# Kernel tuning notes

Hardware: AMD Instinct MI355X
Metric: run time of the kernel (lower is better)

Reference implementation:

```python
import jax, jax.numpy as jnp
import numpy as np


def _glorot(key, shape):
    lim = np.sqrt(6.0 / (shape[-2] + shape[-1])).astype(np.float32)
    return jax.random.uniform(key, shape, jnp.float32, -lim, lim)


def setup_inputs() -> dict:
    key = jax.random.key(0)
    B, F, K, L = 8192, 256, 32768, 4
    H = 2 * F          # CouplingLayer(feat_size, feat_size * 2) hidden width
    half = F // 2      # affine coupling transforms half the features
    ks = jax.random.split(key, 6)
    return {
        "inputs": jax.random.normal(ks[0], (B, F), jnp.float32),
        "W1": _glorot(ks[1], (L, half, H)),
        "b1": jnp.zeros((L, H), jnp.float32),
        "Ws": _glorot(ks[2], (L, H, half)),
        "bs": jnp.zeros((L, half), jnp.float32),
        "Wt": _glorot(ks[3], (L, H, half)),
        "bt": jnp.zeros((L, half), jnp.float32),
        "prior": _glorot(ks[4], (K, F)),  # VQ codebook, GlorotUniform init as in source
    }


def _forward_flow(x, W1, b1, Ws, bs, Wt, bt):
    """Stack of affine coupling layers; returns (y, log|det J|) per sample."""
    L = W1.shape[0]
    jac = jnp.zeros((x.shape[0],), x.dtype)
    for l in range(L):  # small fixed layer count
        xa, xb = jnp.split(x, 2, axis=1)                 # [B, F/2] each
        h = jax.nn.relu(xa @ W1[l] + b1[l])              # [B, 2F]
        s_raw = h @ Ws[l] + bs[l]                        # [B, F/2]
        s = s_raw if l == L - 1 else jnp.tanh(s_raw)     # last layer: tf.identity
        t = h @ Wt[l] + bt[l]
        yb = xb * jnp.exp(s) + t
        jac = jac + jnp.sum(s, axis=1)
        x = jnp.concatenate([yb, xa], axis=1)            # swap halves for mixing
    return x, jac


def reference(inputs, W1, b1, Ws, bs, Wt, bt, prior):
    sg = jax.lax.stop_gradient
    x, jac = _forward_flow(inputs, W1, b1, Ws, bs, Wt, bt)   # [B, F], [B]
    # pairwise squared distance to codebook: [B, K]
    na = jnp.sum(x * x, axis=1, keepdims=True)               # [B, 1]
    nb = jnp.sum(prior * prior, axis=1)[None, :]             # [1, K]
    d = jnp.maximum(na - 2.0 * (x @ prior.T) + nb, 0.0)      # [B, K]
    target_ind = jnp.argmin(d, axis=1)                       # [B]
    target = prior[target_ind]                               # gather, [B, F]
    loss_1 = jnp.mean(jnp.sum((x - sg(target)) ** 2, axis=1) / 2)
    loss_2 = jnp.mean(jnp.sum((sg(x) - target) ** 2, axis=1) / 2)
    loss = loss_1 + 0.25 * loss_2 - jnp.mean(jac)
    return x, loss
```

## Files before the change

kernel.cpp:

```cpp
#include <hip/hip_runtime.h>
#include <hip/hip_fp8.h>
#include <stdint.h>

#define NB     8192
#define NF     256
#define NHALF  128
#define NHID   512
#define NLAY   4
#define NK     32768

#define SX     (1.0f / 16.0f)
#define SP     (256.0f)

typedef __attribute__((ext_vector_type(8))) short bf16x8;
typedef __attribute__((ext_vector_type(4))) float f32x4;
typedef __attribute__((ext_vector_type(2))) long i64x2;

static __device__ __forceinline__ unsigned short f2bf(float f) {
  union { float f; unsigned int u; } v; v.f = f;
  return (unsigned short)((v.u + 0x7FFFu + ((v.u >> 16) & 1u)) >> 16);
}
static __device__ __forceinline__ float bf2f(unsigned short u) {
  union { unsigned int u; float f; } v; v.u = ((unsigned int)u) << 16; return v.f;
}
static __device__ __forceinline__ unsigned char f2fp8(float f) {
  __hip_fp8_e4m3 q(f);
  return (unsigned char)q.__x;
}
static __device__ __forceinline__ float fp82f(unsigned char b) {
  __hip_fp8_e4m3 q; q.__x = b; return (float)q;
}
static __device__ __forceinline__ int kperm(int k) {
  return ((k >> 3) & 3) * 64 + ((k >> 5) << 3) + (k & 7);
}

static __device__ __forceinline__ void load_lds16(const void* g, void* l) {
  __builtin_amdgcn_global_load_lds(
      (const __attribute__((address_space(1))) unsigned int*)g,
      (__attribute__((address_space(3))) unsigned int*)l, 16, 0, 0);
}

static __device__ __forceinline__ unsigned long long packsi(float v, int idx) {
  unsigned int b = __float_as_uint(v);
  b = (b & 0x80000000u) ? ~b : (b | 0x80000000u);
  return ((unsigned long long)b << 32) | (unsigned int)(~(unsigned int)idx);
}

static __device__ __forceinline__ float fast_tanh(float x) {
  const float xc = fminf(fmaxf(x, -15.f), 15.f);
  const float e2 = __expf(2.f * xc);
  return 1.f - 2.f / (e2 + 1.f);
}

static __device__ __forceinline__ int swadr(int kseg, int nrows, int row, int kin) {
  return (kseg * nrows + row) * 64 + (((kin >> 3) ^ (row & 7)) * 8) + (kin & 7);
}

__global__ __launch_bounds__(256, 2)
void flow_all(const float* __restrict__ in,
              const unsigned short* __restrict__ W1T,
              const unsigned short* __restrict__ W2I,
              const float* __restrict__ b1A,
              const float* __restrict__ bsA,
              const float* __restrict__ btA,
              float* __restrict__ xout,
              unsigned char* __restrict__ xf8,
              float* __restrict__ jac)
{
  __shared__ __align__(16) unsigned short Xb[2][16 * 128];
  __shared__ __align__(16) unsigned short Hs[16 * 64];
  __shared__ __align__(16) unsigned short Bs[2][8192];
  __shared__ float jlds[3][16];
  const int tid = threadIdx.x;
  const int lane = tid & 63, wave = tid >> 6;
  const int q = lane >> 4, c = lane & 15;
  const int m0 = blockIdx.x * 16;

  {
    const unsigned short* W1l = W1T;
#pragma unroll
    for (int u = 0; u < 4; u++) {
      const int chb = (u * 4 + wave) * 64;
      const int ch = chb + lane;
      const int kseg = ch >> 9, cs = ch & 511;
      const int row = cs >> 3, cc = (cs & 7) ^ (row & 7);
      load_lds16(W1l + (size_t)row * 128 + kseg * 64 + cc * 8, Bs[0] + chb * 8);
    }
  }

#pragma unroll
  for (int v = 0; v < 4; v++) {
    const int t4 = tid + v * 256;
    const int row = t4 >> 6, f4 = t4 & 63;
    const float4 d = *(const float4*)(in + (size_t)(m0 + row) * NF + f4 * 4);
    unsigned short* dst = Xb[f4 >> 5];
    const int feat = (f4 & 31) * 4;
    const float vals[4] = {d.x, d.y, d.z, d.w};
#pragma unroll
    for (int u = 0; u < 4; u++) {
      const int fe = feat + u;
      dst[swadr(fe >> 6, 16, row, fe & 63)] = f2bf(vals[u]);
    }
  }

  float jr[4] = {0.f, 0.f, 0.f, 0.f};
  bf16x8 af1[4];
  const f32x4 z = {0.f, 0.f, 0.f, 0.f};
  f32x4 acc2[4];

  for (int gs = 0; gs < 96; gs++) {
    __syncthreads();

    if (gs + 1 < 96) {
      const int g2 = gs + 1;
      const int l2 = g2 / 24, s2 = g2 % 24, nc2 = s2 / 3, t2 = s2 % 3;
      unsigned short* dst = Bs[g2 & 1];
      if (t2 == 0) {
        const unsigned short* W1l = W1T + (size_t)l2 * (NHID * NHALF) + (size_t)nc2 * 64 * 128;
#pragma unroll
        for (int u = 0; u < 4; u++) {
          const int chb = (u * 4 + wave) * 64;
          const int ch = chb + lane;
          const int kseg = ch >> 9, cs = ch & 511;
          const int row = cs >> 3, cc = (cs & 7) ^ (row & 7);
          load_lds16(W1l + (size_t)row * 128 + kseg * 64 + cc * 8, dst + chb * 8);
        }
      } else {
        const unsigned short* W2l = W2I + (size_t)l2 * (NF * NHID) + nc2 * 64 + (t2 - 1) * 32;
#pragma unroll
        for (int u = 0; u < 4; u++) {
          const int chb = (u * 4 + wave) * 64;
          const int ch = chb + lane;
          const int row = ch >> 2;
          const int cc = (ch & 3) ^ ((row >> 1) & 3);
          load_lds16(W2l + (size_t)row * NHID + cc * 8, dst + chb * 8);
        }
      }
    }

    const int l = gs / 24, s = gs % 24, nc8 = s / 3, typ = s % 3;
    const unsigned short* B = Bs[gs & 1];
    unsigned short* XA = Xb[l & 1];
    unsigned short* XB = Xb[1 - (l & 1)];

    if (typ == 0) {
      if (s == 0) {
#pragma unroll
        for (int kw = 0; kw < 4; kw++) {
          const int kch = kw * 4 + q;
          af1[kw] = *(const bf16x8*)(XA + ((kch >> 3) * 16 + c) * 64 +
                                     (((kch & 7) ^ (c & 7)) * 8));
        }
#pragma unroll
        for (int j = 0; j < 4; j++) acc2[j] = z;
      }
      f32x4 acc1 = z;
      const int rb = wave * 16 + c;
#pragma unroll
      for (int kw = 0; kw < 4; kw++) {
        const int kseg = kw >> 1, g = (kw & 1) * 4 + q;
        const bf16x8 bf = *(const bf16x8*)(B + (kseg * 64 + rb) * 64 + ((g ^ (rb & 7)) * 8));
        acc1 = __builtin_amdgcn_mfma_f32_16x16x32_bf16(af1[kw], bf, acc1, 0, 0, 0);
      }
      const int hc = wave * 16 + c;
      const float bb = b1A[l * NHID + nc8 * 64 + hc];
#pragma unroll
      for (int r = 0; r < 4; r++) {
        float v = acc1[r] + bb;
        v = v > 0.f ? v : 0.f;
        Hs[swadr(0, 16, 4 * q + r, hc)] = f2bf(v);
      }
    } else {
      const int half = typ - 1;
      const bf16x8 afh = *(const bf16x8*)(Hs + c * 64 + (((half * 4 + q) ^ (c & 7)) * 8));
#pragma unroll
      for (int j = 0; j < 4; j++) {
        const int rb = wave * 64 + 16 * j + c;
        const bf16x8 bf = *(const bf16x8*)(B + rb * 32 + ((q ^ ((rb >> 1) & 3)) * 8));
        acc2[j] = __builtin_amdgcn_mfma_f32_16x16x32_bf16(afh, bf, acc2[j], 0, 0, 0);
      }
    }

    if (s == 23) {
      const int parity = c & 1;
      const int lastl = (l == NLAY - 1);
      const float* bsl = bsA + l * NHALF;
      const float* btl = btA + l * NHALF;
#pragma unroll
      for (int j = 0; j < 4; j++) {
        const int col = wave * 64 + 16 * j + c;
#pragma unroll
        for (int r = 0; r < 4; r++) {
          const float val = acc2[j][r];
          const float oth = __shfl_xor(val, 1);
          if (!parity) {
            const int feat = col >> 1;
            float sv = val + bsl[feat];
            if (!lastl) sv = fast_tanh(sv);
            const float t = oth + btl[feat];
            const int row = 4 * q + r;
            const int xaddr = swadr(feat >> 6, 16, row, feat & 63);
            const float xb = bf2f(XB[xaddr]);
            const float yb = xb * __expf(sv) + t;
            jr[r] += sv;
            XB[xaddr] = f2bf(yb);
            if (l >= 2) {
              const int k = lastl ? feat : (NHALF + feat);
              const size_t grow = (size_t)(m0 + row) * NF;
              xout[grow + k] = yb;
              xf8[(size_t)(m0 + row) * 256 + kperm(k)] = f2fp8(yb * SX);
            }
          }
        }
      }
    }
  }

  float v0[4];
#pragma unroll
  for (int r = 0; r < 4; r++) {
    float v = jr[r];
    v += __shfl_xor(v, 1); v += __shfl_xor(v, 2);
    v += __shfl_xor(v, 4); v += __shfl_xor(v, 8);
    if (c == 0) {
      if (wave) jlds[wave - 1][4 * q + r] = v;
      else v0[r] = v;
    }
  }
  __syncthreads();
  if (wave == 0 && c == 0) {
#pragma unroll
    for (int r = 0; r < 4; r++) {
      const int row = 4 * q + r;
      jac[m0 + row] = v0[r] + jlds[0][row] + jlds[1][row] + jlds[2][row];
    }
  }
}

__global__ __launch_bounds__(256, 2)
void vq_argmax(const unsigned char* __restrict__ X8,
               const unsigned char* __restrict__ P8,
               const float* __restrict__ nbh,
               unsigned long long* __restrict__ gbest)
{
  __shared__ __align__(16) unsigned char Bs[64 * 256];
  const int tid = threadIdx.x;
  const int lane = tid & 63, wave = tid >> 6;
  const int y = blockIdx.x & 15;
  const int m0 = (blockIdx.x >> 4) * 256;
  const int q = lane >> 4, c = lane & 15;
  const int mw = m0 + wave * 64;

  long af[4][8];
#pragma unroll
  for (int i = 0; i < 4; i++) {
    const unsigned char* xr = X8 + (size_t)(mw + 16 * i + c) * 256 + q * 64;
#pragma unroll
    for (int kc2 = 0; kc2 < 4; kc2++) {
      const i64x2 v = *(const i64x2*)(xr + kc2 * 16);
      af[i][2 * kc2] = v.x; af[i][2 * kc2 + 1] = v.y;
    }
  }

  float bestv[16];
  int besti[16];
#pragma unroll
  for (int t = 0; t < 16; t++) { bestv[t] = -1e30f; besti[t] = 0; }

  for (int nt = 0; nt < 32; nt++) {
    const int n0 = y * 2048 + nt * 64;
    if (nt) __syncthreads();
#pragma unroll
    for (int u = 0; u < 4; u++) {
      const int chb = (u * 4 + wave) * 64;
      const int ch = chb + lane;
      const int row = ch >> 4, gslot = ch & 15;
      load_lds16(P8 + (size_t)(n0 + row) * 256 + (gslot ^ (row & 15)) * 16,
                 Bs + chb * 16);
    }
    __syncthreads();

    const f32x4 z = {0.f, 0.f, 0.f, 0.f};
    f32x4 acc[4][4];
#pragma unroll
    for (int i = 0; i < 4; i++)
#pragma unroll
      for (int j = 0; j < 4; j++) acc[i][j] = z;

#pragma unroll
    for (int kc2 = 0; kc2 < 4; kc2++) {
      const int g = q * 4 + kc2;
#pragma unroll
      for (int j = 0; j < 4; j++) {
        const int rb = 16 * j + c;
        const i64x2 b2 = *(const i64x2*)(Bs + rb * 256 + ((g ^ (rb & 15)) * 16));
#pragma unroll
        for (int i = 0; i < 4; i++) {
          acc[i][j] = __builtin_amdgcn_mfma_f32_16x16x32_fp8_fp8(af[i][2 * kc2],     b2.x, acc[i][j], 0, 0, 0);
          acc[i][j] = __builtin_amdgcn_mfma_f32_16x16x32_fp8_fp8(af[i][2 * kc2 + 1], b2.y, acc[i][j], 0, 0, 0);
        }
      }
    }

#pragma unroll
    for (int j = 0; j < 4; j++) {
      const int col = n0 + 16 * j + c;
      const float nb = nbh[col];
#pragma unroll
      for (int i = 0; i < 4; i++)
#pragma unroll
        for (int r = 0; r < 4; r++) {
          const float sc = acc[i][j][r] - nb;
          const int t = i * 4 + r;
          if (sc > bestv[t]) { bestv[t] = sc; besti[t] = col; }
        }
    }
  }

#pragma unroll
  for (int t = 0; t < 16; t++) {
    float lv = bestv[t]; int li = besti[t];
#pragma unroll
    for (int mk = 8; mk >= 1; mk >>= 1) {
      const float ov = __shfl_xor(lv, mk);
      const int oi = __shfl_xor(li, mk);
      if (ov > lv || (ov == lv && oi < li)) { lv = ov; li = oi; }
    }
    if (c == 0) {
      const int row = mw + 16 * (t >> 2) + q * 4 + (t & 3);
      atomicMax(&gbest[row], packsi(lv, li));
    }
  }
}

__global__ void prep_all(const float* __restrict__ W1,
                         const float* __restrict__ Ws,
                         const float* __restrict__ Wt,
                         const float* __restrict__ prior,
                         unsigned short* __restrict__ W1T,
                         unsigned short* __restrict__ W2I,
                         unsigned char* __restrict__ p8,
                         float* __restrict__ nbh,
                         unsigned long long* __restrict__ gbest,
                         float* __restrict__ accum)
{
  __shared__ float ts[64 * 65];
  const int bx = blockIdx.x;
  const int tid = threadIdx.x;
  if (bx < 2048) {
    const int k = bx * 16 + (tid >> 4);
    const int l16 = tid & 15;
    float s = 0.f;
#pragma unroll
    for (int v = 0; v < 4; v++) {
      const int off = (v * 16 + l16) * 4;
      const float4 d = *(const float4*)(prior + (size_t)k * NF + off);
      uchar4 o;
      o.x = f2fp8(d.x * SP); o.y = f2fp8(d.y * SP);
      o.z = f2fp8(d.z * SP); o.w = f2fp8(d.w * SP);
      *(uchar4*)(p8 + (size_t)k * 256 + kperm(off)) = o;
      const float q0 = fp82f(o.x), q1 = fp82f(o.y), q2 = fp82f(o.z), q3 = fp82f(o.w);
      s += q0 * q0 + q1 * q1 + q2 * q2 + q3 * q3;
    }
#pragma unroll
    for (int mk = 8; mk >= 1; mk >>= 1) s += __shfl_xor(s, mk);
    if (l16 == 0) nbh[k] = 0.5f * s * (SX / SP);
  } else if (bx < 2112) {
    const int job = bx - 2048;
    const int l = job >> 4, t = job & 15;
    const int k0 = (t >> 3) * 64, n0 = (t & 7) * 64;
    const float* src = W1 + (size_t)l * NHALF * NHID;
#pragma unroll
    for (int v = 0; v < 16; v++) {
      const int e = tid + v * 256;
      const int kk = e >> 6, nn = e & 63;
      ts[kk * 65 + nn] = src[(size_t)(k0 + kk) * NHID + n0 + nn];
    }
    __syncthreads();
    unsigned short* dst = W1T + (size_t)l * NHID * NHALF;
#pragma unroll
    for (int v = 0; v < 16; v++) {
      const int e = tid + v * 256;
      const int nn = e >> 6, kk = e & 63;
      dst[(size_t)(n0 + nn) * NHALF + k0 + kk] = f2bf(ts[kk * 65 + nn]);
    }
  } else if (bx < 2240) {
    const int job = bx - 2112;
    const int l = job >> 5, rem = job & 31;
    const int b = rem >> 4;
    const int k0 = ((rem >> 1) & 7) * 64;
    const int f0 = (rem & 1) * 64;
    const float* src = (b ? Wt : Ws) + (size_t)l * NHID * NHALF;
#pragma unroll
    for (int v = 0; v < 16; v++) {
      const int e = tid + v * 256;
      const int kk = e >> 6, nn = e & 63;
      ts[kk * 65 + nn] = src[(size_t)(k0 + kk) * NHALF + f0 + nn];
    }
    __syncthreads();
#pragma unroll
    for (int v = 0; v < 16; v++) {
      const int e = tid + v * 256;
      const int nn = e >> 6, kk = e & 63;
      W2I[((size_t)l * NF + 2 * (f0 + nn) + b) * NHID + k0 + kk] = f2bf(ts[kk * 65 + nn]);
    }
  } else {
    const int idx = (bx - 2240) * 256 + tid;
    if (idx < NB) gbest[idx] = 0ull;
    if (idx < 2) accum[idx] = 0.f;
  }
}

__global__ void vq_finalize(const float* __restrict__ X,
                            const float* __restrict__ prior,
                            const unsigned long long* __restrict__ gbest,
                            const float* __restrict__ jac,
                            float* __restrict__ accum)
{
  const int wave = threadIdx.x >> 6, lane = threadIdx.x & 63;
  const int gw = blockIdx.x * 4 + wave;
  float accd = 0.f, accj = 0.f;
  for (int r = 0; r < 8; r++) {
    const int row = gw * 8 + r;
    const unsigned int idx = ~(unsigned int)(gbest[row]);
    const float* x = X + (size_t)row * NF;
    const float* p = prior + (size_t)idx * NF;
#pragma unroll
    for (int u = 0; u < 4; u++) {
      const int d = lane + u * 64;
      const float df = x[d] - p[d];
      accd += df * df;
    }
    if (lane == 0) accj += jac[row];
  }
#pragma unroll
  for (int mk = 32; mk >= 1; mk >>= 1) {
    accd += __shfl_xor(accd, mk);
    accj += __shfl_xor(accj, mk);
  }
  __shared__ float sd[4], sj[4];
  if (lane == 0) { sd[wave] = accd; sj[wave] = accj; }
  __syncthreads();
  if (threadIdx.x == 0) {
    atomicAdd(&accum[0], sd[0] + sd[1] + sd[2] + sd[3]);
    atomicAdd(&accum[1], sj[0] + sj[1] + sj[2] + sj[3]);
  }
}

__global__ void finalize_loss(const float* __restrict__ acc, float* __restrict__ loss) {
  if (threadIdx.x == 0 && blockIdx.x == 0)
    loss[0] = 1.25f * (0.5f * acc[0] / (float)NB) - acc[1] / (float)NB;
}

extern "C" void kernel_launch(void* const* d_in, const int* in_sizes, int n_in,
                              void* d_out, int out_size, void* d_ws, size_t ws_size,
                              hipStream_t stream)
{
  (void)in_sizes; (void)n_in; (void)out_size; (void)ws_size;
  const float* inputs = (const float*)d_in[0];
  const float* W1 = (const float*)d_in[1];
  const float* b1 = (const float*)d_in[2];
  const float* Ws = (const float*)d_in[3];
  const float* bs = (const float*)d_in[4];
  const float* Wt = (const float*)d_in[5];
  const float* bt = (const float*)d_in[6];
  const float* prior = (const float*)d_in[7];

  char* p = (char*)d_ws;
  auto alloc = [&](size_t bytes) { char* r = p; p += (bytes + 255) & ~(size_t)255; return r; };
  unsigned short* W1T  = (unsigned short*)alloc((size_t)NLAY * NHID * NHALF * 2);
  unsigned short* W2I  = (unsigned short*)alloc((size_t)NLAY * NF * NHID * 2);
  unsigned char* P8    = (unsigned char*)alloc((size_t)NK * 256);
  float* NBH           = (float*)alloc((size_t)NK * 4);
  unsigned char* XF8   = (unsigned char*)alloc((size_t)NB * 256);
  float* JAC           = (float*)alloc((size_t)NB * 4);
  unsigned long long* GBEST = (unsigned long long*)alloc((size_t)NB * 8);
  float* ACC           = (float*)alloc(256);

  float* xout = (float*)d_out;
  float* loss = xout + (size_t)NB * NF;

  prep_all<<<dim3(2272), 256, 0, stream>>>(
      W1, Ws, Wt, prior, W1T, W2I, P8, NBH, GBEST, ACC);

  flow_all<<<dim3(NB / 16), 256, 0, stream>>>(
      inputs, W1T, W2I, b1, bs, bt, xout, XF8, JAC);

  vq_argmax<<<dim3(32 * 16), 256, 0, stream>>>(XF8, P8, NBH, GBEST);
  vq_finalize<<<dim3(256), 256, 0, stream>>>(xout, prior, GBEST, JAC, ACC);
  finalize_loss<<<1, 1, 0, stream>>>(ACC, loss);
}
```

Measured before the change: 292.6 us.

## Triple-buffer flow weight staging, double-buffer VQ codebook tiles, fuse loss finalize

flow_all moves from two LDS weight buffers to three. It prefetches two segments ahead and uses a partial vmcnt wait before the barrier, so global-to-LDS loads overlap more compute. The biases are cached in LDS. vq_argmax double-buffers its codebook tiles and preloads the norms into registers. The finalize_loss launch is removed by having the last vq_finalize block compute the loss through an atomic counter. The extra LDS raises per-block usage and may cut occupancy.

Measured after the change: 285.7 us. -2.4%, faster.

```diff
diff --git a/kernel.cpp b/kernel.cpp
--- a/kernel.cpp
+++ b/kernel.cpp
@@ -54,6 +54,36 @@
 
 static __device__ __forceinline__ int swadr(int kseg, int nrows, int row, int kin) {
   return (kseg * nrows + row) * 64 + (((kin >> 3) ^ (row & 7)) * 8) + (kin & 7);
+}
+
+static __device__ __forceinline__ void stage_seg(
+    int g, unsigned short* dst,
+    const unsigned short* __restrict__ W1T,
+    const unsigned short* __restrict__ W2I,
+    int wave, int lane)
+{
+  const int l = g / 24, s = g % 24, nc = s / 3, t = s % 3;
+  if (t == 0) {
+    const unsigned short* W1l = W1T + (size_t)l * (NHID * NHALF) + (size_t)nc * 64 * 128;
+#pragma unroll
+    for (int u = 0; u < 4; u++) {
+      const int chb = (u * 4 + wave) * 64;
+      const int ch = chb + lane;
+      const int kseg = ch >> 9, cs = ch & 511;
+      const int row = cs >> 3, cc = (cs & 7) ^ (row & 7);
+      load_lds16(W1l + (size_t)row * 128 + kseg * 64 + cc * 8, dst + chb * 8);
+    }
+  } else {
+    const unsigned short* W2l = W2I + (size_t)l * (NF * NHID) + nc * 64 + (t - 1) * 32;
+#pragma unroll
+    for (int u = 0; u < 4; u++) {
+      const int chb = (u * 4 + wave) * 64;
+      const int ch = chb + lane;
+      const int row = ch >> 2;
+      const int cc = (ch & 3) ^ ((row >> 1) & 3);
+      load_lds16(W2l + (size_t)row * NHID + cc * 8, dst + chb * 8);
+    }
+  }
 }
 
 __global__ __launch_bounds__(256, 2)
@@ -69,24 +99,17 @@
 {
   __shared__ __align__(16) unsigned short Xb[2][16 * 128];
   __shared__ __align__(16) unsigned short Hs[16 * 64];
-  __shared__ __align__(16) unsigned short Bs[2][8192];
+  __shared__ __align__(16) unsigned short Bs[3][8192];
+  __shared__ float b1s[NLAY * NHID];
+  __shared__ float bss[NLAY * NHALF];
+  __shared__ float bts[NLAY * NHALF];
   __shared__ float jlds[3][16];
   const int tid = threadIdx.x;
   const int lane = tid & 63, wave = tid >> 6;
   const int q = lane >> 4, c = lane & 15;
   const int m0 = blockIdx.x * 16;
 
-  {
-    const unsigned short* W1l = W1T;
-#pragma unroll
-    for (int u = 0; u < 4; u++) {
-      const int chb = (u * 4 + wave) * 64;
-      const int ch = chb + lane;
-      const int kseg = ch >> 9, cs = ch & 511;
-      const int row = cs >> 3, cc = (cs & 7) ^ (row & 7);
-      load_lds16(W1l + (size_t)row * 128 + kseg * 64 + cc * 8, Bs[0] + chb * 8);
-    }
-  }
+  stage_seg(0, Bs[0], W1T, W2I, wave, lane);
 
 #pragma unroll
   for (int v = 0; v < 4; v++) {
@@ -103,43 +126,31 @@
     }
   }
 
+#pragma unroll
+  for (int v = 0; v < 8; v++) b1s[tid + v * 256] = b1A[tid + v * 256];
+#pragma unroll
+  for (int v = 0; v < 2; v++) {
+    bss[tid + v * 256] = bsA[tid + v * 256];
+    bts[tid + v * 256] = btA[tid + v * 256];
+  }
+
+  stage_seg(1, Bs[1], W1T, W2I, wave, lane);
+
   float jr[4] = {0.f, 0.f, 0.f, 0.f};
   bf16x8 af1[4];
   const f32x4 z = {0.f, 0.f, 0.f, 0.f};
   f32x4 acc2[4];
 
   for (int gs = 0; gs < 96; gs++) {
-    __syncthreads();
-
-    if (gs + 1 < 96) {
-      const int g2 = gs + 1;
-      const int l2 = g2 / 24, s2 = g2 % 24, nc2 = s2 / 3, t2 = s2 % 3;
-      unsigned short* dst = Bs[g2 & 1];
-      if (t2 == 0) {
-        const unsigned short* W1l = W1T + (size_t)l2 * (NHID * NHALF) + (size_t)nc2 * 64 * 128;
-#pragma unroll
-        for (int u = 0; u < 4; u++) {
-          const int chb = (u * 4 + wave) * 64;
-          const int ch = chb + lane;
-          const int kseg = ch >> 9, cs = ch & 511;
-          const int row = cs >> 3, cc = (cs & 7) ^ (row & 7);
-          load_lds16(W1l + (size_t)row * 128 + kseg * 64 + cc * 8, dst + chb * 8);
-        }
-      } else {
-        const unsigned short* W2l = W2I + (size_t)l2 * (NF * NHID) + nc2 * 64 + (t2 - 1) * 32;
-#pragma unroll
-        for (int u = 0; u < 4; u++) {
-          const int chb = (u * 4 + wave) * 64;
-          const int ch = chb + lane;
-          const int row = ch >> 2;
-          const int cc = (ch & 3) ^ ((row >> 1) & 3);
-          load_lds16(W2l + (size_t)row * NHID + cc * 8, dst + chb * 8);
-        }
-      }
-    }
+    if (gs < 95)
+      asm volatile("s_waitcnt vmcnt(4) lgkmcnt(0)\n\ts_barrier" ::: "memory");
+    else
+      asm volatile("s_waitcnt vmcnt(0) lgkmcnt(0)\n\ts_barrier" ::: "memory");
+
+    if (gs + 2 < 96) stage_seg(gs + 2, Bs[(gs + 2) % 3], W1T, W2I, wave, lane);
 
     const int l = gs / 24, s = gs % 24, nc8 = s / 3, typ = s % 3;
-    const unsigned short* B = Bs[gs & 1];
+    const unsigned short* B = Bs[gs % 3];
     unsigned short* XA = Xb[l & 1];
     unsigned short* XB = Xb[1 - (l & 1)];
 
@@ -163,7 +174,7 @@
         acc1 = __builtin_amdgcn_mfma_f32_16x16x32_bf16(af1[kw], bf, acc1, 0, 0, 0);
       }
       const int hc = wave * 16 + c;
-      const float bb = b1A[l * NHID + nc8 * 64 + hc];
+      const float bb = b1s[l * NHID + nc8 * 64 + hc];
 #pragma unroll
       for (int r = 0; r < 4; r++) {
         float v = acc1[r] + bb;
@@ -184,8 +195,8 @@
     if (s == 23) {
       const int parity = c & 1;
       const int lastl = (l == NLAY - 1);
-      const float* bsl = bsA + l * NHALF;
-      const float* btl = btA + l * NHALF;
+      const float* bsl = bss + l * NHALF;
+      const float* btl = bts + l * NHALF;
 #pragma unroll
       for (int j = 0; j < 4; j++) {
         const int col = wave * 64 + 16 * j + c;
@@ -243,7 +254,7 @@
                const float* __restrict__ nbh,
                unsigned long long* __restrict__ gbest)
 {
-  __shared__ __align__(16) unsigned char Bs[64 * 256];
+  __shared__ __align__(16) unsigned char Bs[2][64 * 256];
   const int tid = threadIdx.x;
   const int lane = tid & 63, wave = tid >> 6;
   const int y = blockIdx.x & 15;
@@ -267,19 +278,40 @@
 #pragma unroll
   for (int t = 0; t < 16; t++) { bestv[t] = -1e30f; besti[t] = 0; }
 
-  for (int nt = 0; nt < 32; nt++) {
-    const int n0 = y * 2048 + nt * 64;
-    if (nt) __syncthreads();
+  {
+    const int n0s = y * 2048;
 #pragma unroll
     for (int u = 0; u < 4; u++) {
       const int chb = (u * 4 + wave) * 64;
       const int ch = chb + lane;
       const int row = ch >> 4, gslot = ch & 15;
-      load_lds16(P8 + (size_t)(n0 + row) * 256 + (gslot ^ (row & 15)) * 16,
-                 Bs + chb * 16);
-    }
+      load_lds16(P8 + (size_t)(n0s + row) * 256 + (gslot ^ (row & 15)) * 16,
+                 Bs[0] + chb * 16);
+    }
+  }
+
+  for (int nt = 0; nt < 32; nt++) {
+    const int n0 = y * 2048 + nt * 64;
     __syncthreads();
 
+    float nbr[4];
+#pragma unroll
+    for (int j = 0; j < 4; j++) nbr[j] = nbh[n0 + 16 * j + c];
+
+    if (nt + 1 < 32) {
+      const int n0s = n0 + 64;
+      unsigned char* dst = Bs[(nt + 1) & 1];
+#pragma unroll
+      for (int u = 0; u < 4; u++) {
+        const int chb = (u * 4 + wave) * 64;
+        const int ch = chb + lane;
+        const int row = ch >> 4, gslot = ch & 15;
+        load_lds16(P8 + (size_t)(n0s + row) * 256 + (gslot ^ (row & 15)) * 16,
+                   dst + chb * 16);
+      }
+    }
+
+    const unsigned char* Bt = Bs[nt & 1];
     const f32x4 z = {0.f, 0.f, 0.f, 0.f};
     f32x4 acc[4][4];
 #pragma unroll
@@ -293,7 +325,7 @@
 #pragma unroll
       for (int j = 0; j < 4; j++) {
         const int rb = 16 * j + c;
-        const i64x2 b2 = *(const i64x2*)(Bs + rb * 256 + ((g ^ (rb & 15)) * 16));
+        const i64x2 b2 = *(const i64x2*)(Bt + rb * 256 + ((g ^ (rb & 15)) * 16));
 #pragma unroll
         for (int i = 0; i < 4; i++) {
           acc[i][j] = __builtin_amdgcn_mfma_f32_16x16x32_fp8_fp8(af[i][2 * kc2],     b2.x, acc[i][j], 0, 0, 0);
@@ -305,7 +337,7 @@
 #pragma unroll
     for (int j = 0; j < 4; j++) {
       const int col = n0 + 16 * j + c;
-      const float nb = nbh[col];
+      const float nb = nbr[j];
 #pragma unroll
       for (int i = 0; i < 4; i++)
 #pragma unroll
@@ -407,7 +439,7 @@
   } else {
     const int idx = (bx - 2240) * 256 + tid;
     if (idx < NB) gbest[idx] = 0ull;
-    if (idx < 2) accum[idx] = 0.f;
+    if (idx < 4) accum[idx] = 0.f;
   }
 }
 
@@ -415,7 +447,8 @@
                             const float* __restrict__ prior,
                             const unsigned long long* __restrict__ gbest,
                             const float* __restrict__ jac,
-                            float* __restrict__ accum)
+                            float* __restrict__ accum,
+                            float* __restrict__ loss)
 {
   const int wave = threadIdx.x >> 6, lane = threadIdx.x & 63;
   const int gw = blockIdx.x * 4 + wave;
@@ -444,12 +477,14 @@
   if (threadIdx.x == 0) {
     atomicAdd(&accum[0], sd[0] + sd[1] + sd[2] + sd[3]);
     atomicAdd(&accum[1], sj[0] + sj[1] + sj[2] + sj[3]);
-  }
-}
-
-__global__ void finalize_loss(const float* __restrict__ acc, float* __restrict__ loss) {
-  if (threadIdx.x == 0 && blockIdx.x == 0)
-    loss[0] = 1.25f * (0.5f * acc[0] / (float)NB) - acc[1] / (float)NB;
+    __threadfence();
+    const unsigned int t = atomicAdd((unsigned int*)&accum[2], 1u);
+    if (t == 255u) {
+      const float d = atomicAdd(&accum[0], 0.f);
+      const float jv = atomicAdd(&accum[1], 0.f);
+      loss[0] = 1.25f * (0.5f * d / (float)NB) - jv / (float)NB;
+    }
+  }
 }
 
 extern "C" void kernel_launch(void* const* d_in, const int* in_sizes, int n_in,
@@ -487,6 +522,5 @@
       inputs, W1T, W2I, b1, bs, bt, xout, XF8, JAC);
 
   vq_argmax<<<dim3(32 * 16), 256, 0, stream>>>(XF8, P8, NBH, GBEST);
-  vq_finalize<<<dim3(256), 256, 0, stream>>>(xout, prior, GBEST, JAC, ACC);
-  finalize_loss<<<1, 1, 0, stream>>>(ACC, loss);
-}
+  vq_finalize<<<dim3(256), 256, 0, stream>>>(xout, prior, GBEST, JAC, ACC, loss);
+}
```
